# Kernel tuning notes

Hardware: AMD Instinct MI355X
Metric: run time of the kernel (lower is better)

The kernel has to match this reference:

```python
import jax, jax.numpy as jnp
import numpy as np

B, T, C, D, H, NT, ND = 256, 64, 4880, 128, 1024, 101, 10


def setup_inputs() -> dict:
    key = jax.random.key(0)
    ks = jax.random.split(key, 12)
    Hs = (jax.random.uniform(ks[0], (B, C, T)) < 0.005).astype(jnp.float32)  # multi-hot codes per visit
    timestamps = jnp.arange(NT, dtype=jnp.float32) * 0.1  # grid matches rk4 step_size=0.1
    last_idx = jax.random.randint(ks[1], (B,), 0, NT)
    llm_idx = jax.random.randint(ks[2], (B, ND), 0, C)
    eps = jax.random.normal(ks[3], (B, H), dtype=jnp.float32)
    s = lambda k, sh, fan: (jax.random.normal(k, sh, dtype=jnp.float32) / np.float32(np.sqrt(fan)))
    return dict(
        Hs=Hs, timestamps=timestamps, last_idx=last_idx, llm_idx=llm_idx, eps=eps,
        emb_table=s(ks[4], (C, D), D),
        gru_Wih=s(ks[5], (3 * H, D), D),
        gru_Whh=s(ks[6], (3 * H, H), H),
        gru_bih=jnp.zeros((3 * H,), jnp.float32),
        gru_bhh=jnp.zeros((3 * H,), jnp.float32),
        attn_w=s(ks[7], (H,), H),
        fc_mu_W=s(ks[8], (H, H), H), fc_mu_b=jnp.zeros((H,), jnp.float32),
        fc_var_W=s(ks[9], (H, H), H), fc_var_b=jnp.zeros((H,), jnp.float32),
        ode_Whz=s(ks[10], (H, H), H),
        ode_Whn=s(ks[11], (H, H), H),
    )


def reference(Hs, timestamps, last_idx, llm_idx, eps, emb_table, gru_Wih, gru_Whh,
              gru_bih, gru_bhh, attn_w, fc_mu_W, fc_mu_b, fc_var_W, fc_var_b,
              ode_Whz, ode_Whn):
    # ---- Encoder (vectorized over patients) ----
    visit_emb = jnp.einsum('bct,cd->btd', Hs, emb_table)  # H.T @ X per patient: [B,T,D]
    gi = visit_emb @ gru_Wih.T + gru_bih                  # precompute input gates [B,T,3H]

    def gru_step(h, gi_t):
        gh = h @ gru_Whh.T + gru_bhh
        i_r, i_z, i_n = jnp.split(gi_t, 3, axis=-1)
        h_r, h_z, h_n = jnp.split(gh, 3, axis=-1)
        r = jax.nn.sigmoid(i_r + h_r)
        z = jax.nn.sigmoid(i_z + h_z)
        n = jnp.tanh(i_n + r * h_n)
        h_new = (1.0 - z) * n + z * h
        return h_new, h_new

    h0 = jnp.zeros((Hs.shape[0], gru_Whh.shape[1]), dtype=visit_emb.dtype)
    _, hs = jax.lax.scan(gru_step, h0, jnp.swapaxes(gi, 0, 1))  # [T,B,H]
    hs = jnp.swapaxes(hs, 0, 1)                                  # [B,T,H]

    alpha = jax.nn.softmax(hs @ attn_w, axis=-1)                 # [B,T]
    henc = jnp.einsum('bt,bth->bh', alpha, hs)                   # [B,H]

    # ---- VAE reparameterization ----
    mu = henc @ fc_mu_W.T + fc_mu_b
    log_var = henc @ fc_var_W.T + fc_var_b
    z0 = mu + jnp.exp(0.5 * log_var) * eps                       # [B,H]

    # ---- GRU-ODE integrated with RK4 (one step per grid interval, dt=0.1) ----
    def f(h):
        zz = jax.nn.sigmoid(h @ ode_Whz.T)
        nn_ = jnp.tanh((zz * h) @ ode_Whn.T)
        return (1.0 - zz) * (nn_ - h)

    def rk4(h, dt):
        k1 = f(h)
        k2 = f(h + 0.5 * dt * k1)
        k3 = f(h + 0.5 * dt * k2)
        k4 = f(h + dt * k3)
        hn = h + (dt / 6.0) * (k1 + 2.0 * k2 + 2.0 * k3 + k4)
        return hn, hn

    dts = timestamps[1:] - timestamps[:-1]
    _, traj = jax.lax.scan(rk4, z0, dts)                         # [NT-1,B,H]
    pred_z = jnp.concatenate([z0[None], traj], axis=0)           # [NT,B,H]
    pred_z = jnp.swapaxes(pred_z, 0, 1)                          # [B,NT,H]

    # ---- per-patient last-visit state + LLM diagnosis mask ----
    last_visit_emb = pred_z[jnp.arange(pred_z.shape[0]), last_idx]  # [B,H]
    mask = jnp.zeros((Hs.shape[0], C), jnp.float32).at[
        jnp.arange(Hs.shape[0])[:, None], llm_idx].set(1.0)          # [B,4880]
    return last_visit_emb, mask
```

## Files before the change

### kernel.cpp

```cpp
#include <hip/hip_runtime.h>
#include <hip/hip_bf16.h>

#define DEVI __device__ __forceinline__

namespace {

constexpr int nB = 256, nT = 64, nC = 4880, nD = 128, nH = 1024, nNT = 101, nND = 10;

typedef __attribute__((ext_vector_type(8))) short bfrag;
typedef __attribute__((ext_vector_type(4))) float ffrag;
typedef __attribute__((ext_vector_type(4))) unsigned int uvec4;

DEVI ffrag mfma16(bfrag a, bfrag b, ffrag c) {
  return __builtin_amdgcn_mfma_f32_16x16x32_bf16(a, b, c, 0, 0, 0);
}

DEVI unsigned short f2b(float x) {
  __hip_bfloat16 h = __float2bfloat16(x);
  return *reinterpret_cast<unsigned short*>(&h);
}
DEVI float b2f(unsigned short u) {
  __hip_bfloat16 h;
  *reinterpret_cast<unsigned short*>(&h) = u;
  return __bfloat162float(h);
}
DEVI float sigm(float x) { return 1.f / (1.f + expf(-x)); }

template<int NS>
DEVI void mm_stream(ffrag (&acc)[NS],
                    const unsigned short* __restrict__ A, int lda, int K,
                    const unsigned short* const (&Wp)[NS], int ldw,
                    int m0, int n0, int tid, int lane, int mq, int nq,
                    unsigned short* As, unsigned short* Ws) {
  const int r = tid >> 3, blk = tid & 7;
  const int wrOff = (r * 8 + (blk ^ (r & 7))) * 8;
  const int ra = mq * 16 + (lane & 15);
  const int rw = nq * 16 + (lane & 15);
  const int q = lane >> 4;
  const int nc = K >> 6;

  uvec4 va = *(const uvec4*)(A + (size_t)(m0 + r) * lda + blk * 8);
  uvec4 vw[NS];
#pragma unroll
  for (int s = 0; s < NS; ++s)
    vw[s] = *(const uvec4*)(Wp[s] + (size_t)(n0 + r) * ldw + blk * 8);
  *(uvec4*)(As + wrOff) = va;
#pragma unroll
  for (int s = 0; s < NS; ++s) *(uvec4*)(Ws + s * 2048 + wrOff) = vw[s];

  for (int ci = 0; ci < nc; ++ci) {
    __syncthreads();
    const int cur = ci & 1;
    const bool more = (ci + 1) < nc;
    if (more) {
      const int k0 = (ci + 1) << 6;
      va = *(const uvec4*)(A + (size_t)(m0 + r) * lda + k0 + blk * 8);
#pragma unroll
      for (int s = 0; s < NS; ++s)
        vw[s] = *(const uvec4*)(Wp[s] + (size_t)(n0 + r) * ldw + k0 + blk * 8);
    }
    const unsigned short* Ab = As + cur * 2048;
    const unsigned short* Wb = Ws + cur * (NS * 2048);
#pragma unroll
    for (int kk = 0; kk < 2; ++kk) {
      bfrag af = *(const bfrag*)(Ab + (ra * 8 + ((kk * 4 + q) ^ (ra & 7))) * 8);
#pragma unroll
      for (int s = 0; s < NS; ++s) {
        bfrag wf = *(const bfrag*)(Wb + s * 2048 + (rw * 8 + ((kk * 4 + q) ^ (rw & 7))) * 8);
        acc[s] = mfma16(af, wf, acc[s]);
      }
    }
    if (more) {
      const int nx = cur ^ 1;
      *(uvec4*)(As + nx * 2048 + wrOff) = va;
#pragma unroll
      for (int s = 0; s < NS; ++s)
        *(uvec4*)(Ws + nx * (NS * 2048) + s * 2048 + wrOff) = vw[s];
    }
  }
  __syncthreads();
}

__global__ void k_cvt(const float* __restrict__ s, unsigned short* __restrict__ d, int n) {
  int i = blockIdx.x * blockDim.x + threadIdx.x;
  float4 v = ((const float4*)s)[i];
  unsigned int u0 = (unsigned int)f2b(v.x) | ((unsigned int)f2b(v.y) << 16);
  unsigned int u1 = (unsigned int)f2b(v.z) | ((unsigned int)f2b(v.w) << 16);
  ((uint2*)d)[i] = make_uint2(u0, u1);
}

__global__ void k_mask(const int* __restrict__ llm, float* __restrict__ outm) {
  int c = blockIdx.x * 256 + threadIdx.x;
  int b = blockIdx.y;
  if (c >= nC) return;
  const int* lr = llm + b * nND;
  float v = 0.f;
#pragma unroll
  for (int i = 0; i < nND; ++i) v = (lr[i] == c) ? 1.f : v;
  outm[(size_t)b * nC + c] = v;
}

__global__ void k_embed(const float* __restrict__ Hs, const float* __restrict__ emb,
                        unsigned short* __restrict__ ve) {
  __shared__ float tile[4][16][128];
  const int b = blockIdx.x;
  const int tid = threadIdx.x;
  const int w = tid >> 6, lane = tid & 63;
  float* tw = &tile[w][0][0];
  for (int i = lane; i < 16 * 128; i += 64) tw[i] = 0.f;
  const float* hb = Hs + (size_t)b * nC * nT;
  const int tq = w * 16;
  const int tl = lane & 15;
  const int co = lane >> 4;
  for (int cb = 0; cb < nC; cb += 4) {
    const int c = cb + co;
    float v = hb[(size_t)c * nT + tq + tl];
    unsigned long long m = __ballot(v != 0.f);
    while (m) {
      const int p = __ffsll(m) - 1;
      m &= m - 1;
      const int cc = cb + (p >> 4);
      const int tt = p & 15;
      const float vv = __shfl(v, p);
      const float* er = emb + (size_t)cc * nD;
      tile[w][tt][lane]      += vv * er[lane];
      tile[w][tt][lane + 64] += vv * er[lane + 64];
    }
  }
  for (int rr = 0; rr < 16; ++rr) {
    unsigned short* o = ve + ((size_t)b * nT + tq + rr) * nD;
    o[lane]      = f2b(tile[w][rr][lane]);
    o[lane + 64] = f2b(tile[w][rr][lane + 64]);
  }
}

__global__ __launch_bounds__(256) void k_gru(
    int t,
    const unsigned short* __restrict__ hib, const float* __restrict__ hif,
    const unsigned short* __restrict__ ve,
    const unsigned short* __restrict__ Whh, const unsigned short* __restrict__ Wih,
    const float* __restrict__ bih, const float* __restrict__ bhh,
    float* __restrict__ hof, unsigned short* __restrict__ hob,
    unsigned short* __restrict__ hsb) {
  __shared__ __align__(16) unsigned short As[2 * 2048];
  __shared__ __align__(16) unsigned short Ws[2 * 3 * 2048];
  const int tid = threadIdx.x, lane = tid & 63, w = tid >> 6;
  const int mq = w & 1, nq = w >> 1;
  const int m0 = blockIdx.x * 32, n0 = blockIdx.y * 32;

  ffrag acc1[3] = {};
  const unsigned short* const Wp1[3] = {Whh, Whh + (size_t)nH * nH, Whh + (size_t)2 * nH * nH};
  mm_stream<3>(acc1, hib, nH, nH, Wp1, nH, m0, n0, tid, lane, mq, nq, As, Ws);
  ffrag acc2[3] = {};
  const unsigned short* const Wp2[3] = {Wih, Wih + (size_t)nH * nD, Wih + (size_t)2 * nH * nD};
  mm_stream<3>(acc2, ve + (size_t)t * nD, nT * nD, nD, Wp2, nD, m0, n0, tid, lane, mq, nq, As, Ws);

  const int col = n0 + nq * 16 + (lane & 15);
  const int rb = m0 + mq * 16 + ((lane >> 4) << 2);
  const float b_r = bih[col] + bhh[col];
  const float b_z = bih[nH + col] + bhh[nH + col];
  const float bi_n = bih[2 * nH + col];
  const float bh_n = bhh[2 * nH + col];
#pragma unroll
  for (int i = 0; i < 4; ++i) {
    const int row = rb + i;
    const size_t idx = (size_t)row * nH + col;
    const float rr = sigm(acc1[0][i] + acc2[0][i] + b_r);
    const float zv = sigm(acc1[1][i] + acc2[1][i] + b_z);
    const float nn = tanhf(acc2[2][i] + bi_n + rr * (acc1[2][i] + bh_n));
    const float hold = hif[idx];
    const float hnew = (1.f - zv) * nn + zv * hold;
    hof[idx] = hnew;
    const unsigned short h16 = f2b(hnew);
    hob[idx] = h16;
    hsb[((size_t)row * nT + t) * nH + col] = h16;
  }
}

__global__ void k_attn(const unsigned short* __restrict__ hsb,
                       const float* __restrict__ aw,
                       unsigned short* __restrict__ hencb) {
  __shared__ float sc[nT];
  __shared__ float al[nT];
  const int b = blockIdx.x;
  const int tid = threadIdx.x;
  const int w = tid >> 6, lane = tid & 63;
  for (int t = w; t < nT; t += 4) {
    const unsigned short* hr = hsb + ((size_t)b * nT + t) * nH;
    float s = 0.f;
    for (int i = lane; i < nH; i += 64) s += b2f(hr[i]) * aw[i];
#pragma unroll
    for (int o = 32; o > 0; o >>= 1) s += __shfl_xor(s, o);
    if (lane == 0) sc[t] = s;
  }
  __syncthreads();
  if (tid < nT) {
    float v = sc[tid];
    float mx = v;
#pragma unroll
    for (int o = 32; o > 0; o >>= 1) mx = fmaxf(mx, __shfl_xor(mx, o));
    float e = expf(v - mx);
    float su = e;
#pragma unroll
    for (int o = 32; o > 0; o >>= 1) su += __shfl_xor(su, o);
    al[tid] = e / su;
  }
  __syncthreads();
  for (int col = tid; col < nH; col += 256) {
    float a = 0.f;
    for (int t = 0; t < nT; ++t) a += al[t] * b2f(hsb[((size_t)b * nT + t) * nH + col]);
    hencb[(size_t)b * nH + col] = f2b(a);
  }
}

__global__ __launch_bounds__(256) void k_vae(
    const unsigned short* __restrict__ hencb,
    const unsigned short* __restrict__ Wmu, const unsigned short* __restrict__ Wvar,
    const float* __restrict__ bmu, const float* __restrict__ bvar,
    const float* __restrict__ eps,
    float* __restrict__ hf, unsigned short* __restrict__ hb,
    const int* __restrict__ lidx, float* __restrict__ out) {
  __shared__ __align__(16) unsigned short As[2 * 2048];
  __shared__ __align__(16) unsigned short Ws[2 * 2 * 2048];
  const int tid = threadIdx.x, lane = tid & 63, w = tid >> 6;
  const int mq = w & 1, nq = w >> 1;
  const int m0 = blockIdx.x * 32, n0 = blockIdx.y * 32;
  ffrag acc[2] = {};
  const unsigned short* const Wp[2] = {Wmu, Wvar};
  mm_stream<2>(acc, hencb, nH, nH, Wp, nH, m0, n0, tid, lane, mq, nq, As, Ws);
  const int col = n0 + nq * 16 + (lane & 15);
  const int rb = m0 + mq * 16 + ((lane >> 4) << 2);
#pragma unroll
  for (int i = 0; i < 4; ++i) {
    const int row = rb + i;
    const size_t idx = (size_t)row * nH + col;
    const float mu = acc[0][i] + bmu[col];
    const float lv = acc[1][i] + bvar[col];
    const float z0 = mu + expf(0.5f * lv) * eps[idx];
    hf[idx] = z0;
    hb[idx] = f2b(z0);
    if (lidx[row] == 0) out[idx] = z0;
  }
}

DEVI void rb_bar(unsigned* c, unsigned tgt) {
  asm volatile("s_waitcnt vmcnt(0)" ::: "memory");
  __syncthreads();
  if (threadIdx.x == 0) {
    __hip_atomic_fetch_add(c, 1u, __ATOMIC_RELAXED, __HIP_MEMORY_SCOPE_AGENT);
    while (__hip_atomic_load(c, __ATOMIC_RELAXED, __HIP_MEMORY_SCOPE_AGENT) < tgt)
      __builtin_amdgcn_s_sleep(2);
  }
  __syncthreads();
}

DEVI void stageW(const unsigned short* __restrict__ Wg, int n0, int tid,
                 unsigned short* Ws) {
  const int r = tid >> 3, b0 = tid & 7;
  const unsigned short* src = Wg + (size_t)(n0 + r) * nH;
  unsigned short* dst = Ws + r * 1024;
#pragma unroll
  for (int t2 = 0; t2 < 16; ++t2) {
    const int blk = b0 + 8 * t2;
    *(uvec4*)(dst + (blk ^ (r & 7)) * 8) = *(const uvec4*)(src + blk * 8);
  }
}

DEVI void ld8w(uvec4 (&d)[8], const unsigned short* p) {
  asm volatile(
      "global_load_dwordx4 %0, %8, off sc0\n\t"
      "global_load_dwordx4 %1, %8, off offset:64 sc0\n\t"
      "global_load_dwordx4 %2, %8, off offset:128 sc0\n\t"
      "global_load_dwordx4 %3, %8, off offset:192 sc0\n\t"
      "global_load_dwordx4 %4, %8, off offset:256 sc0\n\t"
      "global_load_dwordx4 %5, %8, off offset:320 sc0\n\t"
      "global_load_dwordx4 %6, %8, off offset:384 sc0\n\t"
      "global_load_dwordx4 %7, %8, off offset:448 sc0\n\t"
      "s_waitcnt vmcnt(0)"
      : "=&v"(d[0]), "=&v"(d[1]), "=&v"(d[2]), "=&v"(d[3]),
        "=&v"(d[4]), "=&v"(d[5]), "=&v"(d[6]), "=&v"(d[7])
      : "v"(p)
      : "memory");
}

DEVI ffrag mm_l2(const unsigned short* ag, const unsigned short* wrow,
                 int q, int rx) {
  ffrag a0 = {0.f, 0.f, 0.f, 0.f}, a1 = {0.f, 0.f, 0.f, 0.f};
#pragma unroll
  for (int g = 0; g < 4; ++g) {
    uvec4 A[8];
    ld8w(A, ag + g * 256);
#pragma unroll
    for (int k8 = 0; k8 < 8; k8 += 2) {
      const int kk = g * 8 + k8;
      a0 = mfma16(*(const bfrag*)&A[k8],
                  *(const bfrag*)(wrow + (((kk * 4 + q) ^ rx) * 8)), a0);
      a1 = mfma16(*(const bfrag*)&A[k8 + 1],
                  *(const bfrag*)(wrow + ((((kk + 1) * 4 + q) ^ rx) * 8)), a1);
    }
  }
  return a0 + a1;
}

DEVI void pack_store(const float v[4], unsigned short* pkw, int lane,
                     unsigned short* dst ) {
  const int cl = lane & 15, r0l = (lane >> 4) << 2;
#pragma unroll
  for (int i = 0; i < 4; ++i) pkw[(r0l + i) * 16 + cl] = f2b(v[i]);
  asm volatile("s_waitcnt lgkmcnt(0)" ::: "memory");
  __builtin_amdgcn_sched_barrier(0);
  const int pr = lane >> 2, pc = (lane & 3) << 2;
  *(unsigned long long*)(dst + pr * nH + pc) =
      *(const unsigned long long*)(pkw + pr * 16 + pc);
}

__global__ __launch_bounds__(256, 1) void k_ode_persist(
    const unsigned short* __restrict__ Wz_g, const unsigned short* __restrict__ Wn_g,
    const float* __restrict__ h0f, unsigned short* xb, unsigned short* gbuf,
    const float* __restrict__ ts, const int* __restrict__ lidx,
    float* __restrict__ out, unsigned* ctr) {
  __shared__ __align__(16) unsigned short Wz[32 * nH];
  __shared__ __align__(16) unsigned short Wn[32 * nH];
  __shared__ __align__(16) unsigned short pk[4][16][16];
  __shared__ unsigned rank_sh;
  const int tid = threadIdx.x, lane = tid & 63, w = tid >> 6;
  const int mq = w & 1, nq = w >> 1;

  unsigned xcd;
  asm volatile("s_getreg_b32 %0, hwreg(HW_REG_XCC_ID)" : "=s"(xcd));
  if (tid == 0)
    rank_sh = __hip_atomic_fetch_add(ctr + 512 + (xcd & 7) * 16, 1u,
                                     __ATOMIC_RELAXED, __HIP_MEMORY_SCOPE_AGENT);
  __syncthreads();
  const int i = (int)(xcd & 7);
  const int j = (int)(rank_sh & 31);
  const int m0 = i * 32, n0 = j * 32;

  stageW(Wz_g, n0, tid, Wz);
  stageW(Wn_g, n0, tid, Wn);

  const int col = n0 + nq * 16 + (lane & 15);
  const int row0 = m0 + mq * 16 + ((lane >> 4) << 2);
  const int arow = m0 + mq * 16 + (lane & 15);
  const int q = lane >> 4;
  const int rw = nq * 16 + (lane & 15);
  const int rx = rw & 7;
  const unsigned short* wzrow = Wz + rw * nH;
  const unsigned short* wnrow = Wn + rw * nH;
  const unsigned short* axb = xb + (size_t)arow * nH + q * 8;
  const unsigned short* agb = gbuf + (size_t)arow * nH + q * 8;
  unsigned short* pkw = &pk[w][0][0];
  unsigned short* gdst = gbuf + (size_t)(m0 + mq * 16) * nH + n0 + nq * 16;
  unsigned short* xdst = xb + (size_t)(m0 + mq * 16) * nH + n0 + nq * 16;

  float hb[4], xv[4], ka[4];
  int lst[4];
#pragma unroll
  for (int ii = 0; ii < 4; ++ii) {
    hb[ii] = h0f[(size_t)(row0 + ii) * nH + col];
    xv[ii] = hb[ii];
    lst[ii] = lidx[row0 + ii];
  }
  unsigned* myc = ctr + i * 64;
  unsigned ph = 0;
  __syncthreads();

  for (int s = 0; s < nNT - 1; ++s) {
    const float dt = ts[s + 1] - ts[s];
#pragma unroll 1
    for (int stg = 0; stg < 4; ++stg) {
      ffrag acc = mm_l2(axb, wzrow, q, rx);
      float zv[4], gv[4];
#pragma unroll
      for (int ii = 0; ii < 4; ++ii) {
        zv[ii] = sigm(acc[ii]);
        gv[ii] = zv[ii] * xv[ii];
      }
      pack_store(gv, pkw, lane, gdst);
      ph += 32; rb_bar(myc, ph);
      acc = mm_l2(agb, wnrow, q, rx);
#pragma unroll
      for (int ii = 0; ii < 4; ++ii) {
        const float nn = tanhf(acc[ii]);
        const float fv = (1.f - zv[ii]) * (nn - xv[ii]);
        if (stg == 0)      { ka[ii] = fv;        xv[ii] = hb[ii] + 0.5f * dt * fv; }
        else if (stg == 1) { ka[ii] += 2.f * fv; xv[ii] = hb[ii] + 0.5f * dt * fv; }
        else if (stg == 2) { ka[ii] += 2.f * fv; xv[ii] = hb[ii] + dt * fv; }
        else {
          const float hn = hb[ii] + (dt * (1.f / 6.f)) * (ka[ii] + fv);
          hb[ii] = hn; xv[ii] = hn;
          if (lst[ii] == s + 1) out[(size_t)(row0 + ii) * nH + col] = hn;
        }
      }
      pack_store(xv, pkw, lane, xdst);
      ph += 32; rb_bar(myc, ph);
    }
  }
}

}

extern "C" void kernel_launch(void* const* d_in, const int* in_sizes, int n_in,
                              void* d_out, int out_size, void* d_ws, size_t ws_size,
                              hipStream_t stream) {
  const float* Hs   = (const float*)d_in[0];
  const float* ts   = (const float*)d_in[1];
  const int*   lidx = (const int*)d_in[2];
  const int*   llm  = (const int*)d_in[3];
  const float* eps  = (const float*)d_in[4];
  const float* emb  = (const float*)d_in[5];
  const float* Wih  = (const float*)d_in[6];
  const float* Whh  = (const float*)d_in[7];
  const float* bih  = (const float*)d_in[8];
  const float* bhh  = (const float*)d_in[9];
  const float* aw   = (const float*)d_in[10];
  const float* Wmu  = (const float*)d_in[11];
  const float* bmu  = (const float*)d_in[12];
  const float* Wvar = (const float*)d_in[13];
  const float* bvar = (const float*)d_in[14];
  const float* Whz  = (const float*)d_in[15];
  const float* Whn  = (const float*)d_in[16];

  float* out_last = (float*)d_out;
  float* out_mask = out_last + (size_t)nB * nH;

  char* p = (char*)d_ws;
  auto alloc = [&](size_t bytes) {
    void* r = p; p += (bytes + 255) & ~(size_t)255; return r;
  };
  unsigned short* Whh_b  = (unsigned short*)alloc((size_t)3 * nH * nH * 2);
  unsigned short* Wih_b  = (unsigned short*)alloc((size_t)3 * nH * nD * 2);
  unsigned short* Wmu_b  = (unsigned short*)alloc((size_t)nH * nH * 2);
  unsigned short* Wvar_b = (unsigned short*)alloc((size_t)nH * nH * 2);
  unsigned short* Whz_b  = (unsigned short*)alloc((size_t)nH * nH * 2);
  unsigned short* Whn_b  = (unsigned short*)alloc((size_t)nH * nH * 2);
  unsigned short* ve_b   = (unsigned short*)alloc((size_t)nB * nT * nD * 2);
  unsigned short* hs_b   = (unsigned short*)alloc((size_t)nB * nT * nH * 2);
  float* h0f             = (float*)alloc((size_t)nB * nH * 4);
  float* h1f             = (float*)alloc((size_t)nB * nH * 4);
  unsigned short* h0b    = (unsigned short*)alloc((size_t)nB * nH * 2);
  unsigned short* h1b    = (unsigned short*)alloc((size_t)nB * nH * 2);
  unsigned short* gb     = (unsigned short*)alloc((size_t)nB * nH * 2);
  unsigned short* hencb  = (unsigned short*)alloc((size_t)nB * nH * 2);
  unsigned* ctr          = (unsigned*)alloc(4096);

  hipMemsetAsync(h0f, 0, (size_t)nB * nH * 4, stream);
  hipMemsetAsync(h0b, 0, (size_t)nB * nH * 2, stream);
  hipMemsetAsync(ctr, 0, 4096, stream);

  auto cvt = [&](const float* s, unsigned short* d, int n) {
    k_cvt<<<n / 1024, 256, 0, stream>>>(s, d, n);
  };
  cvt(Whh, Whh_b, 3 * nH * nH);
  cvt(Wih, Wih_b, 3 * nH * nD);
  cvt(Wmu, Wmu_b, nH * nH);
  cvt(Wvar, Wvar_b, nH * nH);
  cvt(Whz, Whz_b, nH * nH);
  cvt(Whn, Whn_b, nH * nH);

  k_embed<<<nB, 256, 0, stream>>>(Hs, emb, ve_b);
  k_mask<<<dim3((nC + 255) / 256, nB), 256, 0, stream>>>(llm, out_mask);

  const dim3 gg(nB / 32, nH / 32);
  for (int t = 0; t < nT; ++t) {
    const unsigned short* hib = (t & 1) ? h1b : h0b;
    const float* hif = (t & 1) ? h1f : h0f;
    unsigned short* hob = (t & 1) ? h0b : h1b;
    float* hof = (t & 1) ? h0f : h1f;
    k_gru<<<gg, 256, 0, stream>>>(t, hib, hif, ve_b, Whh_b, Wih_b, bih, bhh,
                                  hof, hob, hs_b);
  }
  k_attn<<<nB, 256, 0, stream>>>(hs_b, aw, hencb);
  k_vae<<<gg, 256, 0, stream>>>(hencb, Wmu_b, Wvar_b, bmu, bvar, eps,
                                h0f, h0b, lidx, out_last);

  k_ode_persist<<<256, 256, 0, stream>>>(Whz_b, Whn_b, h0f, h0b, gb, ts, lidx,
                                         out_last, ctr);
}
```

Before: 5.610 ms.

## Load GRU operands straight to registers and double-buffer ODE global loads

The GRU step kernel stops staging the hidden state and weight tiles through shared memory and instead has each lane load its MFMA fragments directly from global memory, with no LDS traffic or barriers. Separately, the ODE matmul helper issues global loads for the next K group before computing on the current one, waiting only on the older batch. This aims to hide global-memory latency in the ODE loop and to cut LDS staging and synchronisation cost in the 64 GRU launches. In exchange, the GRU fragment loads are 16-byte strided reads per row with less coalescing, and the prefetching raises register pressure.

```diff
diff --git a/kernel.cpp b/kernel.cpp
--- a/kernel.cpp
+++ b/kernel.cpp
@@ -134,7 +134,7 @@
   }
 }
 
-__global__ __launch_bounds__(256) void k_gru(
+__global__ __launch_bounds__(256) void k_gru2(
     int t,
     const unsigned short* __restrict__ hib, const float* __restrict__ hif,
     const unsigned short* __restrict__ ve,
@@ -142,18 +142,38 @@
     const float* __restrict__ bih, const float* __restrict__ bhh,
     float* __restrict__ hof, unsigned short* __restrict__ hob,
     unsigned short* __restrict__ hsb) {
-  __shared__ __align__(16) unsigned short As[2 * 2048];
-  __shared__ __align__(16) unsigned short Ws[2 * 3 * 2048];
   const int tid = threadIdx.x, lane = tid & 63, w = tid >> 6;
   const int mq = w & 1, nq = w >> 1;
   const int m0 = blockIdx.x * 32, n0 = blockIdx.y * 32;
+  const int arow = m0 + mq * 16 + (lane & 15);
+  const int q = lane >> 4;
+  const int rwl = n0 + nq * 16 + (lane & 15);
+
+  const unsigned short* ah = hib + (size_t)arow * nH + q * 8;
+  const unsigned short* av = ve + ((size_t)arow * nT + t) * nD + q * 8;
+  const unsigned short* w0 = Whh + (size_t)(0 * nH + rwl) * nH + q * 8;
+  const unsigned short* w1 = Whh + (size_t)(1 * nH + rwl) * nH + q * 8;
+  const unsigned short* w2 = Whh + (size_t)(2 * nH + rwl) * nH + q * 8;
+  const unsigned short* v0 = Wih + (size_t)(0 * nH + rwl) * nD + q * 8;
+  const unsigned short* v1 = Wih + (size_t)(1 * nH + rwl) * nD + q * 8;
+  const unsigned short* v2 = Wih + (size_t)(2 * nH + rwl) * nD + q * 8;
 
   ffrag acc1[3] = {};
-  const unsigned short* const Wp1[3] = {Whh, Whh + (size_t)nH * nH, Whh + (size_t)2 * nH * nH};
-  mm_stream<3>(acc1, hib, nH, nH, Wp1, nH, m0, n0, tid, lane, mq, nq, As, Ws);
+#pragma unroll
+  for (int kk = 0; kk < 32; ++kk) {
+    bfrag af = *(const bfrag*)(ah + kk * 32);
+    acc1[0] = mfma16(af, *(const bfrag*)(w0 + kk * 32), acc1[0]);
+    acc1[1] = mfma16(af, *(const bfrag*)(w1 + kk * 32), acc1[1]);
+    acc1[2] = mfma16(af, *(const bfrag*)(w2 + kk * 32), acc1[2]);
+  }
   ffrag acc2[3] = {};
-  const unsigned short* const Wp2[3] = {Wih, Wih + (size_t)nH * nD, Wih + (size_t)2 * nH * nD};
-  mm_stream<3>(acc2, ve + (size_t)t * nD, nT * nD, nD, Wp2, nD, m0, n0, tid, lane, mq, nq, As, Ws);
+#pragma unroll
+  for (int kk = 0; kk < 4; ++kk) {
+    bfrag af = *(const bfrag*)(av + kk * 32);
+    acc2[0] = mfma16(af, *(const bfrag*)(v0 + kk * 32), acc2[0]);
+    acc2[1] = mfma16(af, *(const bfrag*)(v1 + kk * 32), acc2[1]);
+    acc2[2] = mfma16(af, *(const bfrag*)(v2 + kk * 32), acc2[2]);
+  }
 
   const int col = n0 + nq * 16 + (lane & 15);
   const int rb = m0 + mq * 16 + ((lane >> 4) << 2);
@@ -266,7 +286,7 @@
   }
 }
 
-DEVI void ld8w(uvec4 (&d)[8], const unsigned short* p) {
+DEVI void ld8_issue(uvec4 (&d)[8], const unsigned short* p) {
   asm volatile(
       "global_load_dwordx4 %0, %8, off sc0\n\t"
       "global_load_dwordx4 %1, %8, off offset:64 sc0\n\t"
@@ -275,30 +295,48 @@
       "global_load_dwordx4 %4, %8, off offset:256 sc0\n\t"
       "global_load_dwordx4 %5, %8, off offset:320 sc0\n\t"
       "global_load_dwordx4 %6, %8, off offset:384 sc0\n\t"
-      "global_load_dwordx4 %7, %8, off offset:448 sc0\n\t"
-      "s_waitcnt vmcnt(0)"
+      "global_load_dwordx4 %7, %8, off offset:448 sc0"
       : "=&v"(d[0]), "=&v"(d[1]), "=&v"(d[2]), "=&v"(d[3]),
         "=&v"(d[4]), "=&v"(d[5]), "=&v"(d[6]), "=&v"(d[7])
       : "v"(p)
       : "memory");
 }
 
+DEVI void wait_vm8() {
+  asm volatile("s_waitcnt vmcnt(8)" ::: "memory");
+  __builtin_amdgcn_sched_barrier(0);
+}
+DEVI void wait_vm0() {
+  asm volatile("s_waitcnt vmcnt(0)" ::: "memory");
+  __builtin_amdgcn_sched_barrier(0);
+}
+
+#define MM_GROUP(ARR, G)                                                     \
+  _Pragma("unroll")                                                          \
+  for (int k8 = 0; k8 < 8; k8 += 2) {                                        \
+    const int kk = (G) * 8 + k8;                                             \
+    a0 = mfma16(*(const bfrag*)&ARR[k8],                                     \
+                *(const bfrag*)(wrow + (((kk * 4 + q) ^ rx) * 8)), a0);      \
+    a1 = mfma16(*(const bfrag*)&ARR[k8 + 1],                                 \
+                *(const bfrag*)(wrow + ((((kk + 1) * 4 + q) ^ rx) * 8)), a1);\
+  }
+
 DEVI ffrag mm_l2(const unsigned short* ag, const unsigned short* wrow,
                  int q, int rx) {
+  uvec4 A[8], B[8], C[8], D[8];
+  ld8_issue(A, ag);
+  ld8_issue(B, ag + 256);
   ffrag a0 = {0.f, 0.f, 0.f, 0.f}, a1 = {0.f, 0.f, 0.f, 0.f};
-#pragma unroll
-  for (int g = 0; g < 4; ++g) {
-    uvec4 A[8];
-    ld8w(A, ag + g * 256);
-#pragma unroll
-    for (int k8 = 0; k8 < 8; k8 += 2) {
-      const int kk = g * 8 + k8;
-      a0 = mfma16(*(const bfrag*)&A[k8],
-                  *(const bfrag*)(wrow + (((kk * 4 + q) ^ rx) * 8)), a0);
-      a1 = mfma16(*(const bfrag*)&A[k8 + 1],
-                  *(const bfrag*)(wrow + ((((kk + 1) * 4 + q) ^ rx) * 8)), a1);
-    }
-  }
+  wait_vm8();
+  MM_GROUP(A, 0)
+  ld8_issue(C, ag + 512);
+  wait_vm8();
+  MM_GROUP(B, 1)
+  ld8_issue(D, ag + 768);
+  wait_vm8();
+  MM_GROUP(C, 2)
+  wait_vm0();
+  MM_GROUP(D, 3)
   return a0 + a1;
 }
 
@@ -467,8 +505,8 @@
     const float* hif = (t & 1) ? h1f : h0f;
     unsigned short* hob = (t & 1) ? h0b : h1b;
     float* hof = (t & 1) ? h0f : h1f;
-    k_gru<<<gg, 256, 0, stream>>>(t, hib, hif, ve_b, Whh_b, Wih_b, bih, bhh,
-                                  hof, hob, hs_b);
+    k_gru2<<<gg, 256, 0, stream>>>(t, hib, hif, ve_b, Whh_b, Wih_b, bih, bhh,
+                                   hof, hob, hs_b);
   }
   k_attn<<<nB, 256, 0, stream>>>(hs_b, aw, hencb);
   k_vae<<<gg, 256, 0, stream>>>(hencb, Wmu_b, Wvar_b, bmu, bvar, eps,
```

After: 6.000 ms. 7.0% more time.

## Split ODE persistent kernel into 16-row bands with Wz streamed from global

Applied to the files above, without the earlier changes.

The persistent RK4 GRU-ODE kernel now launches 512 blocks of 128 threads instead of 256 blocks of 256 threads. Each block owns a 16-row by 32-column tile, and each 16-row band synchronises on its own counter. Only the Wn slice is staged in LDS. Wz fragments are loaded directly from global/L2 on every stage, which halves LDS per block so two blocks can share a CU. This trades LDS capacity and occupancy for extra L2 weight traffic on every RK4 stage.

```diff
diff --git a/kernel.cpp b/kernel.cpp
--- a/kernel.cpp
+++ b/kernel.cpp
@@ -254,14 +254,14 @@
   __syncthreads();
 }
 
-DEVI void stageW(const unsigned short* __restrict__ Wg, int n0, int tid,
-                 unsigned short* Ws) {
-  const int r = tid >> 3, b0 = tid & 7;
+DEVI void stageW128(const unsigned short* __restrict__ Wg, int n0, int tid,
+                    unsigned short* Ws) {
+  const int r = tid >> 2, b0 = tid & 3;
   const unsigned short* src = Wg + (size_t)(n0 + r) * nH;
   unsigned short* dst = Ws + r * 1024;
 #pragma unroll
-  for (int t2 = 0; t2 < 16; ++t2) {
-    const int blk = b0 + 8 * t2;
+  for (int t2 = 0; t2 < 32; ++t2) {
+    const int blk = b0 + 4 * t2;
     *(uvec4*)(dst + (blk ^ (r & 7)) * 8) = *(const uvec4*)(src + blk * 8);
   }
 }
@@ -283,8 +283,8 @@
       : "memory");
 }
 
-DEVI ffrag mm_l2(const unsigned short* ag, const unsigned short* wrow,
-                 int q, int rx) {
+DEVI ffrag mm_lds(const unsigned short* ag, const unsigned short* wrow,
+                  int q, int rx) {
   ffrag a0 = {0.f, 0.f, 0.f, 0.f}, a1 = {0.f, 0.f, 0.f, 0.f};
 #pragma unroll
   for (int g = 0; g < 4; ++g) {
@@ -302,6 +302,25 @@
   return a0 + a1;
 }
 
+DEVI ffrag mm_gw(const unsigned short* ag, const unsigned short* __restrict__ wg,
+                 int q) {
+  ffrag a0 = {0.f, 0.f, 0.f, 0.f}, a1 = {0.f, 0.f, 0.f, 0.f};
+#pragma unroll
+  for (int g = 0; g < 4; ++g) {
+    uvec4 A[8];
+    ld8w(A, ag + g * 256);
+#pragma unroll
+    for (int k8 = 0; k8 < 8; k8 += 2) {
+      const int kk = g * 8 + k8;
+      a0 = mfma16(*(const bfrag*)&A[k8],
+                  *(const bfrag*)(wg + kk * 32), a0);
+      a1 = mfma16(*(const bfrag*)&A[k8 + 1],
+                  *(const bfrag*)(wg + (kk + 1) * 32), a1);
+    }
+  }
+  return a0 + a1;
+}
+
 DEVI void pack_store(const float v[4], unsigned short* pkw, int lane,
                      unsigned short* dst ) {
   const int cl = lane & 15, r0l = (lane >> 4) << 2;
@@ -314,44 +333,43 @@
       *(const unsigned long long*)(pkw + pr * 16 + pc);
 }
 
-__global__ __launch_bounds__(256, 1) void k_ode_persist(
+__global__ __launch_bounds__(128, 1) void k_ode_persist(
     const unsigned short* __restrict__ Wz_g, const unsigned short* __restrict__ Wn_g,
     const float* __restrict__ h0f, unsigned short* xb, unsigned short* gbuf,
     const float* __restrict__ ts, const int* __restrict__ lidx,
     float* __restrict__ out, unsigned* ctr) {
-  __shared__ __align__(16) unsigned short Wz[32 * nH];
   __shared__ __align__(16) unsigned short Wn[32 * nH];
-  __shared__ __align__(16) unsigned short pk[4][16][16];
+  __shared__ __align__(16) unsigned short pk[2][16][16];
   __shared__ unsigned rank_sh;
-  const int tid = threadIdx.x, lane = tid & 63, w = tid >> 6;
-  const int mq = w & 1, nq = w >> 1;
+  const int tid = threadIdx.x, lane = tid & 63, nq = tid >> 6;
 
   unsigned xcd;
   asm volatile("s_getreg_b32 %0, hwreg(HW_REG_XCC_ID)" : "=s"(xcd));
   if (tid == 0)
-    rank_sh = __hip_atomic_fetch_add(ctr + 512 + (xcd & 7) * 16, 1u,
+    rank_sh = __hip_atomic_fetch_add(ctr + 1024 + (xcd & 7) * 16, 1u,
                                      __ATOMIC_RELAXED, __HIP_MEMORY_SCOPE_AGENT);
   __syncthreads();
-  const int i = (int)(xcd & 7);
-  const int j = (int)(rank_sh & 31);
-  const int m0 = i * 32, n0 = j * 32;
-
-  stageW(Wz_g, n0, tid, Wz);
-  stageW(Wn_g, n0, tid, Wn);
+  const unsigned rk = rank_sh;
+  const int band = (int)((xcd & 7) * 2 + (rk & 1));
+  const int j = (int)((rk >> 1) & 31);
+  const int rb0 = band * 16, n0 = j * 32;
+
+  stageW128(Wn_g, n0, tid, Wn);
 
   const int col = n0 + nq * 16 + (lane & 15);
-  const int row0 = m0 + mq * 16 + ((lane >> 4) << 2);
-  const int arow = m0 + mq * 16 + (lane & 15);
+  const int row0 = rb0 + ((lane >> 4) << 2);
+  const int arow = rb0 + (lane & 15);
   const int q = lane >> 4;
   const int rw = nq * 16 + (lane & 15);
   const int rx = rw & 7;
-  const unsigned short* wzrow = Wz + rw * nH;
+  const int rwl = n0 + nq * 16 + (lane & 15);
   const unsigned short* wnrow = Wn + rw * nH;
+  const unsigned short* wzg = Wz_g + (size_t)rwl * nH + q * 8;
   const unsigned short* axb = xb + (size_t)arow * nH + q * 8;
   const unsigned short* agb = gbuf + (size_t)arow * nH + q * 8;
-  unsigned short* pkw = &pk[w][0][0];
-  unsigned short* gdst = gbuf + (size_t)(m0 + mq * 16) * nH + n0 + nq * 16;
-  unsigned short* xdst = xb + (size_t)(m0 + mq * 16) * nH + n0 + nq * 16;
+  unsigned short* pkw = &pk[nq][0][0];
+  unsigned short* gdst = gbuf + (size_t)rb0 * nH + n0 + nq * 16;
+  unsigned short* xdst = xb + (size_t)rb0 * nH + n0 + nq * 16;
 
   float hb[4], xv[4], ka[4];
   int lst[4];
@@ -361,7 +379,7 @@
     xv[ii] = hb[ii];
     lst[ii] = lidx[row0 + ii];
   }
-  unsigned* myc = ctr + i * 64;
+  unsigned* myc = ctr + band * 64;
   unsigned ph = 0;
   __syncthreads();
 
@@ -369,7 +387,7 @@
     const float dt = ts[s + 1] - ts[s];
 #pragma unroll 1
     for (int stg = 0; stg < 4; ++stg) {
-      ffrag acc = mm_l2(axb, wzrow, q, rx);
+      ffrag acc = mm_gw(axb, wzg, q);
       float zv[4], gv[4];
 #pragma unroll
       for (int ii = 0; ii < 4; ++ii) {
@@ -378,7 +396,7 @@
       }
       pack_store(gv, pkw, lane, gdst);
       ph += 32; rb_bar(myc, ph);
-      acc = mm_l2(agb, wnrow, q, rx);
+      acc = mm_lds(agb, wnrow, q, rx);
 #pragma unroll
       for (int ii = 0; ii < 4; ++ii) {
         const float nn = tanhf(acc[ii]);
@@ -442,11 +460,11 @@
   unsigned short* h1b    = (unsigned short*)alloc((size_t)nB * nH * 2);
   unsigned short* gb     = (unsigned short*)alloc((size_t)nB * nH * 2);
   unsigned short* hencb  = (unsigned short*)alloc((size_t)nB * nH * 2);
-  unsigned* ctr          = (unsigned*)alloc(4096);
+  unsigned* ctr          = (unsigned*)alloc(8192);
 
   hipMemsetAsync(h0f, 0, (size_t)nB * nH * 4, stream);
   hipMemsetAsync(h0b, 0, (size_t)nB * nH * 2, stream);
-  hipMemsetAsync(ctr, 0, 4096, stream);
+  hipMemsetAsync(ctr, 0, 8192, stream);
 
   auto cvt = [&](const float* s, unsigned short* d, int n) {
     k_cvt<<<n / 1024, 256, 0, stream>>>(s, d, n);
@@ -474,6 +492,6 @@
   k_vae<<<gg, 256, 0, stream>>>(hencb, Wmu_b, Wvar_b, bmu, bvar, eps,
                                 h0f, h0b, lidx, out_last);
 
-  k_ode_persist<<<256, 256, 0, stream>>>(Whz_b, Whn_b, h0f, h0b, gb, ts, lidx,
+  k_ode_persist<<<512, 128, 0, stream>>>(Whz_b, Whn_b, h0f, h0b, gb, ts, lidx,
                                          out_last, ctr);
 }
```

New measurement: 8.114 ms. 1.45x slower.

## Replace per-timestep GRU launches with persistent kernel using grid barriers

Applied to the files above, without the earlier changes.

The 64 separate GRU step launches are replaced by a single persistent kernel of 256 blocks. Each block pins its r and z slices of Whh and its Wih slice in LDS, streams the n-gate weights from global memory, and keeps the fp32 hidden state in registers. Rows of the batch are assigned per XCD, and a barrier per XCD group synchronises the time steps. This removes launch overhead and repeated weight reloads, but it depends on all 256 blocks being co-resident and on atomic counter barriers working correctly.

```diff
diff --git a/kernel.cpp b/kernel.cpp
--- a/kernel.cpp
+++ b/kernel.cpp
@@ -134,49 +134,6 @@
   }
 }
 
-__global__ __launch_bounds__(256) void k_gru(
-    int t,
-    const unsigned short* __restrict__ hib, const float* __restrict__ hif,
-    const unsigned short* __restrict__ ve,
-    const unsigned short* __restrict__ Whh, const unsigned short* __restrict__ Wih,
-    const float* __restrict__ bih, const float* __restrict__ bhh,
-    float* __restrict__ hof, unsigned short* __restrict__ hob,
-    unsigned short* __restrict__ hsb) {
-  __shared__ __align__(16) unsigned short As[2 * 2048];
-  __shared__ __align__(16) unsigned short Ws[2 * 3 * 2048];
-  const int tid = threadIdx.x, lane = tid & 63, w = tid >> 6;
-  const int mq = w & 1, nq = w >> 1;
-  const int m0 = blockIdx.x * 32, n0 = blockIdx.y * 32;
-
-  ffrag acc1[3] = {};
-  const unsigned short* const Wp1[3] = {Whh, Whh + (size_t)nH * nH, Whh + (size_t)2 * nH * nH};
-  mm_stream<3>(acc1, hib, nH, nH, Wp1, nH, m0, n0, tid, lane, mq, nq, As, Ws);
-  ffrag acc2[3] = {};
-  const unsigned short* const Wp2[3] = {Wih, Wih + (size_t)nH * nD, Wih + (size_t)2 * nH * nD};
-  mm_stream<3>(acc2, ve + (size_t)t * nD, nT * nD, nD, Wp2, nD, m0, n0, tid, lane, mq, nq, As, Ws);
-
-  const int col = n0 + nq * 16 + (lane & 15);
-  const int rb = m0 + mq * 16 + ((lane >> 4) << 2);
-  const float b_r = bih[col] + bhh[col];
-  const float b_z = bih[nH + col] + bhh[nH + col];
-  const float bi_n = bih[2 * nH + col];
-  const float bh_n = bhh[2 * nH + col];
-#pragma unroll
-  for (int i = 0; i < 4; ++i) {
-    const int row = rb + i;
-    const size_t idx = (size_t)row * nH + col;
-    const float rr = sigm(acc1[0][i] + acc2[0][i] + b_r);
-    const float zv = sigm(acc1[1][i] + acc2[1][i] + b_z);
-    const float nn = tanhf(acc2[2][i] + bi_n + rr * (acc1[2][i] + bh_n));
-    const float hold = hif[idx];
-    const float hnew = (1.f - zv) * nn + zv * hold;
-    hof[idx] = hnew;
-    const unsigned short h16 = f2b(hnew);
-    hob[idx] = h16;
-    hsb[((size_t)row * nT + t) * nH + col] = h16;
-  }
-}
-
 __global__ void k_attn(const unsigned short* __restrict__ hsb,
                        const float* __restrict__ aw,
                        unsigned short* __restrict__ hencb) {
@@ -312,6 +269,126 @@
   const int pr = lane >> 2, pc = (lane & 3) << 2;
   *(unsigned long long*)(dst + pr * nH + pc) =
       *(const unsigned long long*)(pkw + pr * 16 + pc);
+}
+
+DEVI void pack_store2(const float v[4], unsigned short* pkw, int lane,
+                      unsigned short* d1 ,
+                      unsigned short* d2 ) {
+  const int cl = lane & 15, r0l = (lane >> 4) << 2;
+#pragma unroll
+  for (int i = 0; i < 4; ++i) pkw[(r0l + i) * 16 + cl] = f2b(v[i]);
+  asm volatile("s_waitcnt lgkmcnt(0)" ::: "memory");
+  __builtin_amdgcn_sched_barrier(0);
+  const int pr = lane >> 2, pc = (lane & 3) << 2;
+  const unsigned long long val = *(const unsigned long long*)(pkw + pr * 16 + pc);
+  *(unsigned long long*)(d1 + (size_t)pr * nH + pc) = val;
+  *(unsigned long long*)(d2 + (size_t)pr * (nT * nH) + pc) = val;
+}
+
+__global__ __launch_bounds__(256, 1) void k_gru_persist(
+    const unsigned short* __restrict__ Whh_g, const unsigned short* __restrict__ Wih_g,
+    const float* __restrict__ bih, const float* __restrict__ bhh,
+    const unsigned short* __restrict__ ve,
+    unsigned short* hA, unsigned short* hB,
+    unsigned short* hsb, unsigned* ctr) {
+  __shared__ __align__(16) unsigned short Wr[32 * nH];
+  __shared__ __align__(16) unsigned short Wz2[32 * nH];
+  __shared__ __align__(16) unsigned short Wi[96 * nD];
+  __shared__ __align__(16) unsigned short pk[4][16][16];
+  __shared__ unsigned rank_sh;
+  const int tid = threadIdx.x, lane = tid & 63, w = tid >> 6;
+  const int mq = w & 1, nq = w >> 1;
+
+  unsigned xcd;
+  asm volatile("s_getreg_b32 %0, hwreg(HW_REG_XCC_ID)" : "=s"(xcd));
+  if (tid == 0)
+    rank_sh = __hip_atomic_fetch_add(ctr + 1536 + (xcd & 7) * 16, 1u,
+                                     __ATOMIC_RELAXED, __HIP_MEMORY_SCOPE_AGENT);
+  __syncthreads();
+  const int i = (int)(xcd & 7);
+  const int j = (int)(rank_sh & 31);
+  const int m0 = i * 32, n0 = j * 32;
+
+  stageW(Whh_g, n0, tid, Wr);
+  stageW(Whh_g + (size_t)nH * nH, n0, tid, Wz2);
+  for (int idx = tid; idx < 96 * 16; idx += 256) {
+    const int r = idx >> 4, blk = idx & 15;
+    const int gate = r >> 5, rr2 = r & 31;
+    *(uvec4*)(Wi + r * nD + ((blk ^ (r & 7)) * 8)) =
+        *(const uvec4*)(Wih_g + ((size_t)gate * nH + n0 + rr2) * nD + blk * 8);
+  }
+
+  const int col = n0 + nq * 16 + (lane & 15);
+  const int arow = m0 + mq * 16 + (lane & 15);
+  const int q = lane >> 4;
+  const int rw = nq * 16 + (lane & 15);
+  const int rx = rw & 7;
+  const unsigned short* wrr = Wr + rw * nH;
+  const unsigned short* wzr = Wz2 + rw * nH;
+  const unsigned short* wir = Wi + rw * nD;
+  const unsigned short* wiz = Wi + (32 + rw) * nD;
+  const unsigned short* win = Wi + (64 + rw) * nD;
+  const unsigned short* wng = Whh_g + ((size_t)2 * nH + col) * nH + q * 8;
+  const unsigned short* aA = hA + (size_t)arow * nH + q * 8;
+  const unsigned short* aB = hB + (size_t)arow * nH + q * 8;
+  unsigned short* dA = hA + (size_t)(m0 + mq * 16) * nH + n0 + nq * 16;
+  unsigned short* dB = hB + (size_t)(m0 + mq * 16) * nH + n0 + nq * 16;
+  unsigned short* dh = hsb + (size_t)(m0 + mq * 16) * nT * nH + n0 + nq * 16;
+  unsigned short* pkw = &pk[w][0][0];
+  const float b_r = bih[col] + bhh[col];
+  const float b_z = bih[nH + col] + bhh[nH + col];
+  const float bi_n = bih[2 * nH + col];
+  const float bh_n = bhh[2 * nH + col];
+
+  float hf_[4] = {0.f, 0.f, 0.f, 0.f};
+  unsigned* myc = ctr + 1024 + i * 64;
+  unsigned ph = 0;
+  __syncthreads();
+
+#pragma unroll 1
+  for (int t = 0; t < nT; ++t) {
+    const unsigned short* ah = (t & 1) ? aB : aA;
+    unsigned short* dst = (t & 1) ? dA : dB;
+    ffrag ar = {0.f, 0.f, 0.f, 0.f}, az = {0.f, 0.f, 0.f, 0.f},
+          an = {0.f, 0.f, 0.f, 0.f};
+#pragma unroll
+    for (int g = 0; g < 4; ++g) {
+      uvec4 A[8];
+      ld8w(A, ah + g * 256);
+#pragma unroll
+      for (int k8 = 0; k8 < 8; ++k8) {
+        const int kk = g * 8 + k8;
+        const int wo = ((kk * 4 + q) ^ rx) * 8;
+        const bfrag af = *(const bfrag*)&A[k8];
+        ar = mfma16(af, *(const bfrag*)(wrr + wo), ar);
+        az = mfma16(af, *(const bfrag*)(wzr + wo), az);
+        an = mfma16(af, *(const bfrag*)(wng + kk * 32), an);
+      }
+    }
+    ffrag ir = {0.f, 0.f, 0.f, 0.f}, iz = {0.f, 0.f, 0.f, 0.f},
+          in_ = {0.f, 0.f, 0.f, 0.f};
+    const unsigned short* av = ve + ((size_t)arow * nT + t) * nD + q * 8;
+#pragma unroll
+    for (int kk = 0; kk < 4; ++kk) {
+      const bfrag af = *(const bfrag*)(av + kk * 32);
+      const int wo = ((kk * 4 + q) ^ rx) * 8;
+      ir = mfma16(af, *(const bfrag*)(wir + wo), ir);
+      iz = mfma16(af, *(const bfrag*)(wiz + wo), iz);
+      in_ = mfma16(af, *(const bfrag*)(win + wo), in_);
+    }
+    float hv[4];
+#pragma unroll
+    for (int ii = 0; ii < 4; ++ii) {
+      const float rr2 = sigm(ar[ii] + ir[ii] + b_r);
+      const float zv = sigm(az[ii] + iz[ii] + b_z);
+      const float nn = tanhf(in_[ii] + bi_n + rr2 * (an[ii] + bh_n));
+      const float hn2 = (1.f - zv) * nn + zv * hf_[ii];
+      hf_[ii] = hn2;
+      hv[ii] = hn2;
+    }
+    pack_store2(hv, pkw, lane, dst, dh + (size_t)t * nH);
+    ph += 32; rb_bar(myc, ph);
+  }
 }
 
 __global__ __launch_bounds__(256, 1) void k_ode_persist(
@@ -437,16 +514,14 @@
   unsigned short* ve_b   = (unsigned short*)alloc((size_t)nB * nT * nD * 2);
   unsigned short* hs_b   = (unsigned short*)alloc((size_t)nB * nT * nH * 2);
   float* h0f             = (float*)alloc((size_t)nB * nH * 4);
-  float* h1f             = (float*)alloc((size_t)nB * nH * 4);
   unsigned short* h0b    = (unsigned short*)alloc((size_t)nB * nH * 2);
   unsigned short* h1b    = (unsigned short*)alloc((size_t)nB * nH * 2);
   unsigned short* gb     = (unsigned short*)alloc((size_t)nB * nH * 2);
   unsigned short* hencb  = (unsigned short*)alloc((size_t)nB * nH * 2);
-  unsigned* ctr          = (unsigned*)alloc(4096);
-
-  hipMemsetAsync(h0f, 0, (size_t)nB * nH * 4, stream);
+  unsigned* ctr          = (unsigned*)alloc(8192);
+
   hipMemsetAsync(h0b, 0, (size_t)nB * nH * 2, stream);
-  hipMemsetAsync(ctr, 0, 4096, stream);
+  hipMemsetAsync(ctr, 0, 8192, stream);
 
   auto cvt = [&](const float* s, unsigned short* d, int n) {
     k_cvt<<<n / 1024, 256, 0, stream>>>(s, d, n);
@@ -461,16 +536,11 @@
   k_embed<<<nB, 256, 0, stream>>>(Hs, emb, ve_b);
   k_mask<<<dim3((nC + 255) / 256, nB), 256, 0, stream>>>(llm, out_mask);
 
+  k_gru_persist<<<256, 256, 0, stream>>>(Whh_b, Wih_b, bih, bhh, ve_b,
+                                         h0b, h1b, hs_b, ctr);
+
+  k_attn<<<nB, 256, 0, stream>>>(hs_b, aw, hencb);
   const dim3 gg(nB / 32, nH / 32);
-  for (int t = 0; t < nT; ++t) {
-    const unsigned short* hib = (t & 1) ? h1b : h0b;
-    const float* hif = (t & 1) ? h1f : h0f;
-    unsigned short* hob = (t & 1) ? h0b : h1b;
-    float* hof = (t & 1) ? h0f : h1f;
-    k_gru<<<gg, 256, 0, stream>>>(t, hib, hif, ve_b, Whh_b, Wih_b, bih, bhh,
-                                  hof, hob, hs_b);
-  }
-  k_attn<<<nB, 256, 0, stream>>>(hs_b, aw, hencb);
   k_vae<<<gg, 256, 0, stream>>>(hencb, Wmu_b, Wvar_b, bmu, bvar, eps,
                                 h0f, h0b, lidx, out_last);
 
```

Result: faster. 5.392 ms, median of 2 (-3.9%).
